# Kernel optimization log

Hardware: AMD Instinct MI355X
Metric: run time of the kernel (lower is better)

The kernel has to match this reference:

```python
import jax, jax.numpy as jnp
import numpy as np

VOCAB = 50257
D_MODEL = 1024
BATCH = 4
SEQ = 4096


def setup_inputs() -> dict:
    key = jax.random.key(0)
    k_ids, k_w = jax.random.split(key)
    input = jax.random.randint(k_ids, (BATCH, SEQ), 0, VOCAB, dtype=jnp.int32)
    # Linear(vocab, d_model, bias=False) weight: [d_model, vocab]
    W = jax.random.normal(k_w, (D_MODEL, VOCAB), dtype=jnp.float32) * (1.0 / np.sqrt(VOCAB))
    return {"input": input, "W": W}


def reference(input, W):
    # one_hot(input, vocab) @ W.T  ==  gather columns of W
    # out[b, s, :] = W[:, input[b, s]]  -> shape [B, S, d_model]
    return jnp.take(W.T, input, axis=0)
```

## Files before the change

### kernel.cpp

```cpp
#include <hip/hip_runtime.h>
#include <stdint.h>

#define VOCAB   50257
#define DMODEL  1024
#define VWIN    256
#define NB      ((VOCAB + VWIN - 1) / VWIN)
#define DCH     16
#define CAP     1024

typedef __attribute__((address_space(1))) const void* gas_ptr;
typedef __attribute__((address_space(3))) void*       las_ptr;

__global__ __launch_bounds__(256) void gather_kernel(
    const int* __restrict__ ids, const float* __restrict__ W,
    float* __restrict__ out, int n_tokens)
{
    __shared__ float tile[DCH][VWIN + 1];
    __shared__ int   list[CAP];
    __shared__ int   cnt;

    const int vwin = blockIdx.x;
    const int dk   = blockIdx.y * DCH;
    const int v0   = vwin << 8;
    const int tid  = threadIdx.x;
    const int lane = tid & 63;
    const int w    = tid >> 6;

    if (tid == 0) cnt = 0;

    if (vwin != NB - 1) {
#pragma unroll
        for (int r2 = 0; r2 < 4; ++r2) {
            const int row = w * 4 + r2;
            const float* gsrc = W + (size_t)(dk + row) * VOCAB + v0 + lane;
            float* ldst = &tile[row][0];
#pragma unroll
            for (int q = 0; q < 4; ++q) {
                __builtin_amdgcn_global_load_lds(
                    (gas_ptr)(gsrc + q * 64), (las_ptr)(ldst + q * 64),
                    4, 0, 0);
            }
        }
    } else {
        const int limit = VOCAB - v0;
        for (int e = tid; e < DCH * VWIN; e += 256) {
            int r = e >> 8, c = e & 255;
            if (c < limit)
                tile[r][c] = W[(size_t)(dk + r) * VOCAB + v0 + c];
        }
    }

    __syncthreads();

    for (int t = tid; t < n_tokens; t += 256) {
        int id = ids[t];
        if ((id >> 8) == vwin) {
            int pos = atomicAdd(&cnt, 1);
            if (pos < CAP)
                list[pos] = (int)(((uint32_t)(id & 255) << 16) | (uint32_t)t);
        }
    }

    asm volatile("s_waitcnt vmcnt(0)" ::: "memory");
    __syncthreads();

    const int total = min(cnt, CAP);
    const int g = lane >> 2;
    const int j = lane & 3;

    for (int i = w * 16; i < total; i += 64) {
        int idx = i + g;
        if (idx < total) {
            uint32_t packed = (uint32_t)list[idx];
            int t   = (int)(packed & 0xFFFFu);
            int col = (int)(packed >> 16);
            float4 v;
            v.x = tile[j * 4 + 0][col];
            v.y = tile[j * 4 + 1][col];
            v.z = tile[j * 4 + 2][col];
            v.w = tile[j * 4 + 3][col];
            *(float4*)(out + (size_t)t * DMODEL + dk + j * 4) = v;
        }
    }
}

extern "C" void kernel_launch(void* const* d_in, const int* in_sizes, int n_in,
                              void* d_out, int out_size, void* d_ws, size_t ws_size,
                              hipStream_t stream) {
    const int*   ids = (const int*)d_in[0];
    const float* W   = (const float*)d_in[1];
    float*       out = (float*)d_out;
    (void)d_ws; (void)ws_size;

    const int n_tokens = in_sizes[0];

    dim3 grid(NB, DMODEL / DCH);
    gather_kernel<<<grid, 256, 0, stream>>>(ids, W, out, n_tokens);
}
```

Measured before the change: 398.7 us.

## Double-buffer 16 d-chunks per block to amortize token scan and overlap loads

Each block now covers 16 consecutive DCH row-chunks (256 d-rows) instead of one, so the scan over all token ids that builds the per-window list runs once per 256 rows rather than once per 16. W tiles are staged into two LDS buffers with global_load_lds, mixing 16-byte and 4-byte transfers under a skewed, misalignment-aware LDS layout, and loading the next chunk overlaps emitting the current one. Block size goes from 256 to 512 threads. The costs are far fewer blocks (a 16x smaller grid along y), fragile vmcnt-based synchronization, and more complex indexing.

Measured after the change: 371.7 us. 6.8% less time.

```diff
diff --git a/kernel.cpp b/kernel.cpp
--- a/kernel.cpp
+++ b/kernel.cpp
@@ -6,53 +6,60 @@
 #define VWIN    256
 #define NB      ((VOCAB + VWIN - 1) / VWIN)
 #define DCH     16
+#define NT      16
+#define DQ      (DCH * NT)
 #define CAP     1024
+
+#define LSTRIDE 272
+__device__ __forceinline__ int lidx(int r, int k) {
+    return r * LSTRIDE + ((r >> 2) << 2) + k;
+}
+#define LDS_FLOATS 4352
 
 typedef __attribute__((address_space(1))) const void* gas_ptr;
 typedef __attribute__((address_space(3))) void*       las_ptr;
 
-__global__ __launch_bounds__(256) void gather_kernel(
+__global__ __launch_bounds__(512) void gather_kernel(
     const int* __restrict__ ids, const float* __restrict__ W,
     float* __restrict__ out, int n_tokens)
 {
-    __shared__ float tile[DCH][VWIN + 1];
+    __shared__ float tile[2][LDS_FLOATS];
     __shared__ int   list[CAP];
     __shared__ int   cnt;
 
     const int vwin = blockIdx.x;
-    const int dk   = blockIdx.y * DCH;
+    const int dq0  = blockIdx.y * DQ;
     const int v0   = vwin << 8;
     const int tid  = threadIdx.x;
     const int lane = tid & 63;
     const int w    = tid >> 6;
 
+    const bool tail = (vwin == NB - 1);
+
     if (tid == 0) cnt = 0;
 
-    if (vwin != NB - 1) {
+    auto stage = [&](int buf, int t) {
 #pragma unroll
-        for (int r2 = 0; r2 < 4; ++r2) {
-            const int row = w * 4 + r2;
-            const float* gsrc = W + (size_t)(dk + row) * VOCAB + v0 + lane;
-            float* ldst = &tile[row][0];
-#pragma unroll
-            for (int q = 0; q < 4; ++q) {
-                __builtin_amdgcn_global_load_lds(
-                    (gas_ptr)(gsrc + q * 64), (las_ptr)(ldst + q * 64),
-                    4, 0, 0);
-            }
+        for (int rr = 0; rr < 2; ++rr) {
+            const int row  = w * 2 + rr;
+            const int grow = dq0 + t * DCH + row;
+            const int mis  = row & 3;
+            const size_t gbase = (size_t)grow * VOCAB + v0;
+            __builtin_amdgcn_global_load_lds(
+                (gas_ptr)(W + gbase - mis + (size_t)lane * 4),
+                (las_ptr)(&tile[buf][lidx(row, 0)]), 16, 0, 0);
+            __builtin_amdgcn_global_load_lds(
+                (gas_ptr)(W + gbase + 192 + lane),
+                (las_ptr)(&tile[buf][lidx(row, 192 + mis)]), 4, 0, 0);
         }
-    } else {
-        const int limit = VOCAB - v0;
-        for (int e = tid; e < DCH * VWIN; e += 256) {
-            int r = e >> 8, c = e & 255;
-            if (c < limit)
-                tile[r][c] = W[(size_t)(dk + r) * VOCAB + v0 + c];
-        }
-    }
+    };
 
-    __syncthreads();
+    if (!tail) { stage(0, 0); stage(1, 1); }
 
-    for (int t = tid; t < n_tokens; t += 256) {
+    asm volatile("s_waitcnt lgkmcnt(0)" ::: "memory");
+    __builtin_amdgcn_s_barrier();
+
+    for (int t = tid; t < n_tokens; t += 512) {
         int id = ids[t];
         if ((id >> 8) == vwin) {
             int pos = atomicAdd(&cnt, 1);
@@ -60,26 +67,53 @@
                 list[pos] = (int)(((uint32_t)(id & 255) << 16) | (uint32_t)t);
         }
     }
-
-    asm volatile("s_waitcnt vmcnt(0)" ::: "memory");
-    __syncthreads();
+    asm volatile("s_waitcnt lgkmcnt(0)" ::: "memory");
+    __builtin_amdgcn_s_barrier();
 
     const int total = min(cnt, CAP);
-    const int g = lane >> 2;
-    const int j = lane & 3;
 
-    for (int i = w * 16; i < total; i += 64) {
-        int idx = i + g;
-        if (idx < total) {
-            uint32_t packed = (uint32_t)list[idx];
-            int t   = (int)(packed & 0xFFFFu);
+    auto emit_tile = [&](int buf, int t) {
+        const int dk = dq0 + t * DCH;
+        const int g = lane >> 2;
+        const int j = lane & 3;
+        for (int i = w * 16 + g; i < total; i += 128) {
+            uint32_t packed = (uint32_t)list[i];
+            int tok = (int)(packed & 0xFFFFu);
             int col = (int)(packed >> 16);
             float4 v;
-            v.x = tile[j * 4 + 0][col];
-            v.y = tile[j * 4 + 1][col];
-            v.z = tile[j * 4 + 2][col];
-            v.w = tile[j * 4 + 3][col];
-            *(float4*)(out + (size_t)t * DMODEL + dk + j * 4) = v;
+            v.x = tile[buf][lidx(4 * j + 0, col + 0)];
+            v.y = tile[buf][lidx(4 * j + 1, col + 1)];
+            v.z = tile[buf][lidx(4 * j + 2, col + 2)];
+            v.w = tile[buf][lidx(4 * j + 3, col + 3)];
+            *(float4*)(out + (size_t)tok * DMODEL + dk + j * 4) = v;
+        }
+    };
+
+    if (!tail) {
+        for (int t = 0; t < NT; ++t) {
+            const int cur = t & 1;
+            if (t + 1 < NT) asm volatile("s_waitcnt vmcnt(4)" ::: "memory");
+            else            asm volatile("s_waitcnt vmcnt(0)" ::: "memory");
+            __builtin_amdgcn_s_barrier();
+            asm volatile("" ::: "memory");
+            emit_tile(cur, t);
+            asm volatile("" ::: "memory");
+            __builtin_amdgcn_s_barrier();
+            if (t + 2 < NT) stage(cur, t + 2);
+        }
+    } else {
+        const int limit = VOCAB - v0;
+        for (int t = 0; t < NT; ++t) {
+            const int dk = dq0 + t * DCH;
+            for (int e = tid; e < DCH * VWIN; e += 512) {
+                int r = e >> 8, c = e & 255;
+                if (c < limit)
+                    tile[0][lidx(r, c + (r & 3))] =
+                        W[(size_t)(dk + r) * VOCAB + v0 + c];
+            }
+            __syncthreads();
+            emit_tile(0, t);
+            __syncthreads();
         }
     }
 }
@@ -94,6 +128,6 @@
 
     const int n_tokens = in_sizes[0];
 
-    dim3 grid(NB, DMODEL / DCH);
-    gather_kernel<<<grid, 256, 0, stream>>>(ids, W, out, n_tokens);
+    dim3 grid(NB, DMODEL / DQ);
+    gather_kernel<<<grid, 512, 0, stream>>>(ids, W, out, n_tokens);
 }
```
